# Optimization experiments

Measured on AMD Instinct MI355X. Metric: run time of the kernel, lower is better.

The kernel has to match this reference:

```python
import jax, jax.numpy as jnp
import numpy as np

N = 20000
E = 320000
D = 256
OUT = 256
NEG_SLOPE = 0.2


def setup_inputs() -> dict:
    key = jax.random.key(0)
    ks = jax.random.split(key, 16)
    s = 1.0 / np.sqrt(D)
    x = jax.random.normal(ks[0], (N, D), dtype=jnp.float32)
    edge_index = jax.random.randint(ks[1], (2, E), 0, N, dtype=jnp.int64)
    W1 = jax.random.uniform(ks[2], (D, D), jnp.float32, -s, s)
    W2 = jax.random.uniform(ks[3], (D, D), jnp.float32, -s, s)
    Ws = jax.random.uniform(ks[4], (6, D, D), jnp.float32, -s, s)      # per-layer GATConv lin weight
    a_src = jax.random.uniform(ks[5], (6, D), jnp.float32, -s, s)      # per-layer att_src
    a_dst = jax.random.uniform(ks[6], (6, D), jnp.float32, -s, s)      # per-layer att_dst
    bias = jnp.zeros((6, D), dtype=jnp.float32)                        # per-layer GATConv bias
    W3 = jax.random.uniform(ks[7], (2 * D, OUT), jnp.float32, -s, s)
    return {"x": x, "edge_index": edge_index, "W1": W1, "W2": W2,
            "Ws": Ws, "a_src": a_src, "a_dst": a_dst, "bias": bias, "W3": W3}


def _gat_layer(h, src, dst, W, asrc, adst, b):
    # h: [N, D] -> linear transform
    hw = h @ W                                         # [N, D]
    e_src = hw @ asrc                                  # [N]
    e_dst = hw @ adst                                  # [N]
    e = jax.nn.leaky_relu(e_src[src] + e_dst[dst], NEG_SLOPE)  # [E]
    # softmax over incoming edges per destination node
    m = jax.ops.segment_max(e, dst, num_segments=N)    # [N], -inf for empty segs (unused)
    ee = jnp.exp(e - m[dst])                           # [E]
    denom = jax.ops.segment_sum(ee, dst, num_segments=N)
    alpha = ee / denom[dst]                            # [E]
    msg = alpha[:, None] * hw[src]                     # [E, D]
    out = jax.ops.segment_sum(msg, dst, num_segments=N)  # [N, D]
    return out + b


def reference(x, edge_index, W1, W2, Ws, a_src, a_dst, bias, W3):
    src, dst = edge_index[0], edge_index[1]
    h = x @ W1
    h = h @ W2
    for i in range(6):
        h = _gat_layer(h, src, dst, Ws[i], a_src[i], a_dst[i], bias[i])
    h = jnp.concatenate((h, h), axis=1)   # [N, 2D]
    h = jax.nn.relu(h)
    return h @ W3                          # [N, OUT]
```

## Files before the change

kernel.cpp:

```cpp
#include <hip/hip_runtime.h>
#include <hip/hip_fp16.h>
#include <stdint.h>

#define NNODES 20000
#define EEDGES 320000
#define DD     256
#define NEG_SLOPE 0.2f
#define SCAN_BLOCKS ((NNODES + 255) / 256)
#define ESTR   20480

typedef _Float16 half8 __attribute__((ext_vector_type(8)));
typedef _Float16 half4 __attribute__((ext_vector_type(4)));
typedef float f32x4 __attribute__((ext_vector_type(4)));


__global__ void zero_ints_k(int* __restrict__ p, int n) {
    int i = blockIdx.x * 256 + threadIdx.x;
    if (i < n) p[i] = 0;
}

__global__ void hist_k(const int* __restrict__ dst, int* __restrict__ rowptr) {
    int i = blockIdx.x * 256 + threadIdx.x;
    if (i < EEDGES) atomicAdd(&rowptr[dst[i] + 1], 1);
}

__global__ __launch_bounds__(256) void scan1_k(int* __restrict__ rowptr, int* __restrict__ bsums) {
    __shared__ int buf[256];
    int idx = blockIdx.x * 256 + threadIdx.x;
    int v = (idx < NNODES) ? rowptr[idx + 1] : 0;
    buf[threadIdx.x] = v;
    __syncthreads();
#pragma unroll
    for (int off = 1; off < 256; off <<= 1) {
        int t = (threadIdx.x >= (unsigned)off) ? buf[threadIdx.x - off] : 0;
        __syncthreads();
        buf[threadIdx.x] += t;
        __syncthreads();
    }
    if (idx < NNODES) rowptr[idx + 1] = buf[threadIdx.x];
    if (threadIdx.x == 255) bsums[blockIdx.x] = buf[255];
}

__global__ __launch_bounds__(128) void scan2_k(int* __restrict__ bsums) {
    __shared__ int buf[128];
    int v = (threadIdx.x < SCAN_BLOCKS) ? bsums[threadIdx.x] : 0;
    buf[threadIdx.x] = v;
    __syncthreads();
#pragma unroll
    for (int off = 1; off < 128; off <<= 1) {
        int t = (threadIdx.x >= (unsigned)off) ? buf[threadIdx.x - off] : 0;
        __syncthreads();
        buf[threadIdx.x] += t;
        __syncthreads();
    }
    if (threadIdx.x < SCAN_BLOCKS) bsums[threadIdx.x] = buf[threadIdx.x];
}

__global__ void scan3_k(int* __restrict__ rowptr, const int* __restrict__ bsums,
                        int* __restrict__ cursor) {
    int idx = blockIdx.x * 256 + threadIdx.x;
    if (idx < NNODES) {
        int v = rowptr[idx + 1];
        if (blockIdx.x > 0) { v += bsums[blockIdx.x - 1]; rowptr[idx + 1] = v; }
        if (idx + 1 < NNODES) cursor[idx + 1] = v;
        if (idx == 0) cursor[0] = 0;
    }
}

__global__ void scatter_k(const int* __restrict__ src, const int* __restrict__ dst,
                          int* __restrict__ cursor, int* __restrict__ colsrc) {
    int i = blockIdx.x * 256 + threadIdx.x;
    if (i < EEDGES) {
        int d = dst[i];
        int pos = atomicAdd(&cursor[d], 1);
        colsrc[pos] = src[i];
    }
}


__global__ void cvt_split_k(const float* __restrict__ X, _Float16* __restrict__ Xh,
                            _Float16* __restrict__ Xl, int n) {
    int i = blockIdx.x * 256 + threadIdx.x;
    if (i < n) {
        float v = X[i];
        _Float16 hi = (_Float16)v;
        Xh[i] = hi;
        Xl[i] = (_Float16)(v - (float)hi);
    }
}


template<bool SUM>
__global__ void cvt_w_k(const float* __restrict__ W, _Float16* __restrict__ Wh,
                        _Float16* __restrict__ Wl) {
    int i = blockIdx.x * 256 + threadIdx.x;
    if (i < DD * DD) {
        int k = i >> 8, n = i & 255;
        float v = W[i];
        if (SUM) v += W[i + DD * DD];
        _Float16 hi = (_Float16)v;
        Wh[n * DD + k] = hi;
        Wl[n * DD + k] = (_Float16)(v - (float)hi);
    }
}


template<bool OUT_SPLIT, bool DOTS>
__global__ __launch_bounds__(512, 4) void gemm_k(
    const _Float16* __restrict__ Ah, const _Float16* __restrict__ Al,
    const _Float16* __restrict__ Bh, const _Float16* __restrict__ Bl,
    float* __restrict__ C, _Float16* __restrict__ Ch, _Float16* __restrict__ Cl,
    const float* __restrict__ asrc, const float* __restrict__ adst,
    float* __restrict__ esp, float* __restrict__ edp, int M)
{
    __shared__ _Float16 smem[24576];
    _Float16* sAh = smem;
    _Float16* sAl = smem + 4096;
    _Float16* sBh = smem + 8192;
    _Float16* sBl = smem + 16384;

    const int t = threadIdx.x;
    const int lane = t & 63;
    const int w = t >> 6;
    const int rowBase = blockIdx.y * 64;
    const int colBase = blockIdx.x * 128;
    const int mo = (w & 1) * 32;
    const int no = (w >> 1) * 32;

    const int arow = t >> 3;
    const int slot = t & 7;
    const int swz = (slot ^ (arow & 7)) << 3;

    f32x4 acc[2][2];
#pragma unroll
    for (int m = 0; m < 2; ++m)
#pragma unroll
        for (int n = 0; n < 2; ++n) acc[m][n] = (f32x4){0.f, 0.f, 0.f, 0.f};

    int4 pa_h, pa_l, pb_h0, pb_h1, pb_l0, pb_l1;

#define LOADSTAGE(S) { \
        size_t aoff  = (size_t)(rowBase + arow) * DD + (S) * 64 + slot * 8; \
        size_t boff0 = (size_t)(colBase + arow) * DD + (S) * 64 + slot * 8; \
        size_t boff1 = boff0 + (size_t)64 * DD; \
        pa_h  = *(const int4*)(Ah + aoff); \
        pa_l  = *(const int4*)(Al + aoff); \
        pb_h0 = *(const int4*)(Bh + boff0); \
        pb_h1 = *(const int4*)(Bh + boff1); \
        pb_l0 = *(const int4*)(Bl + boff0); \
        pb_l1 = *(const int4*)(Bl + boff1); \
    }

#define WRITESTAGE() { \
        int da  = arow * 64 + swz; \
        *(int4*)(sAh + da) = pa_h; \
        *(int4*)(sAl + da) = pa_l; \
        *(int4*)(sBh + da) = pb_h0; \
        *(int4*)(sBh + da + 4096) = pb_h1; \
        *(int4*)(sBl + da) = pb_l0; \
        *(int4*)(sBl + da + 4096) = pb_l1; \
    }

    LOADSTAGE(0);
    const int fr = lane & 15;
    const int fq = lane >> 4;

    for (int s = 0; s < 4; ++s) {
        __syncthreads();
        WRITESTAGE();
        __syncthreads();
        if (s < 3) { LOADSTAGE(s + 1); }

#pragma unroll
        for (int kk = 0; kk < 2; ++kk) {
            const int c = kk * 4 + fq;
            half8 ah[2], al[2], bh[2], bl[2];
#pragma unroll
            for (int m = 0; m < 2; ++m) {
                int ra = mo + m * 16 + fr;
                int oa = ra * 64 + ((c ^ (ra & 7)) << 3);
                ah[m] = *(const half8*)(sAh + oa);
                al[m] = *(const half8*)(sAl + oa);
            }
#pragma unroll
            for (int n = 0; n < 2; ++n) {
                int rb = no + n * 16 + fr;
                int ob = rb * 64 + ((c ^ (rb & 7)) << 3);
                bh[n] = *(const half8*)(sBh + ob);
                bl[n] = *(const half8*)(sBl + ob);
            }
#pragma unroll
            for (int m = 0; m < 2; ++m)
#pragma unroll
                for (int n = 0; n < 2; ++n) {
                    acc[m][n] = __builtin_amdgcn_mfma_f32_16x16x32_f16(ah[m], bh[n], acc[m][n], 0, 0, 0);
                    acc[m][n] = __builtin_amdgcn_mfma_f32_16x16x32_f16(ah[m], bl[n], acc[m][n], 0, 0, 0);
                    acc[m][n] = __builtin_amdgcn_mfma_f32_16x16x32_f16(al[m], bh[n], acc[m][n], 0, 0, 0);
                    acc[m][n] = __builtin_amdgcn_mfma_f32_16x16x32_f16(al[m], bl[n], acc[m][n], 0, 0, 0);
                }
        }
    }
#undef LOADSTAGE
#undef WRITESTAGE

    const int ccol = lane & 15;
    const int crq = (lane >> 4) * 4;

    if constexpr (OUT_SPLIT) {
        __syncthreads();
#pragma unroll
        for (int m = 0; m < 2; ++m)
#pragma unroll
            for (int n = 0; n < 2; ++n)
#pragma unroll
                for (int r = 0; r < 4; ++r) {
                    int row = mo + m * 16 + crq + r;
                    int col = no + n * 16 + ccol;
                    float v = acc[m][n][r];
                    _Float16 hi = (_Float16)v;
                    smem[row * 136 + col] = hi;
                    smem[8704 + row * 136 + col] = (_Float16)(v - (float)hi);
                }
        __syncthreads();
#pragma unroll
        for (int i = 0; i < 2; ++i) {
            int slotId = i * 512 + t;
            int srow = slotId >> 4;
            int sc = slotId & 15;
            int grow = rowBase + srow;
            if (grow < M) {
                half8 hv = *(const half8*)(smem + srow * 136 + sc * 8);
                half8 lv = *(const half8*)(smem + 8704 + srow * 136 + sc * 8);
                *(half8*)(Ch + (size_t)grow * DD + colBase + sc * 8) = hv;
                *(half8*)(Cl + (size_t)grow * DD + colBase + sc * 8) = lv;
            }
        }
    } else {
#pragma unroll
        for (int m = 0; m < 2; ++m) {
            int growb = rowBase + mo + m * 16 + crq;
#pragma unroll
            for (int n = 0; n < 2; ++n) {
                int gcol = colBase + no + n * 16 + ccol;
#pragma unroll
                for (int r = 0; r < 4; ++r) {
                    int grow = growb + r;
                    if (grow < M) C[(size_t)grow * DD + gcol] = acc[m][n][r];
                }
            }
        }
    }

    if constexpr (DOTS) {
        float as0 = asrc[colBase + no + ccol];
        float as1 = asrc[colBase + no + 16 + ccol];
        float ad0 = adst[colBase + no + ccol];
        float ad1 = adst[colBase + no + 16 + ccol];
        __syncthreads();
        float* sred = (float*)smem;
        const int cw = w >> 1;
#pragma unroll
        for (int m = 0; m < 2; ++m)
#pragma unroll
            for (int r = 0; r < 4; ++r) {
                float ps = acc[m][0][r] * as0 + acc[m][1][r] * as1;
                float pd = acc[m][0][r] * ad0 + acc[m][1][r] * ad1;
#pragma unroll
                for (int off = 1; off < 16; off <<= 1) {
                    ps += __shfl_xor(ps, off);
                    pd += __shfl_xor(pd, off);
                }
                if (ccol == 0) {
                    int row = mo + m * 16 + crq + r;
                    sred[row * 8 + cw] = ps;
                    sred[512 + row * 8 + cw] = pd;
                }
            }
        __syncthreads();
        if (t < 64) {
            float esb = sred[t * 8 + 0] + sred[t * 8 + 1] + sred[t * 8 + 2] + sred[t * 8 + 3];
            float edb = sred[512 + t * 8 + 0] + sred[512 + t * 8 + 1]
                      + sred[512 + t * 8 + 2] + sred[512 + t * 8 + 3];
            int grow = rowBase + t;
            if (grow < M) {
                esp[(size_t)blockIdx.x * ESTR + grow] = esb;
                edp[(size_t)blockIdx.x * ESTR + grow] = edb;
            }
        }
    }
}


template<bool RELU>
__global__ __launch_bounds__(256) void gat_agg_k(const float* __restrict__ hw,
                                                 const float* __restrict__ es0,
                                                 const float* __restrict__ es1,
                                                 const float* __restrict__ ed0,
                                                 const float* __restrict__ ed1,
                                                 const int* __restrict__ rowptr,
                                                 const int* __restrict__ colsrc,
                                                 float* __restrict__ ealpha,
                                                 const float* __restrict__ bias,
                                                 _Float16* __restrict__ hh,
                                                 _Float16* __restrict__ hl) {
    int wave = threadIdx.x >> 6;
    int lane = threadIdx.x & 63;
    int node = blockIdx.x * 4 + wave;
    if (node >= NNODES) return;
    int start = rowptr[node], end = rowptr[node + 1];
    int deg = end - start;
    float edd = ed0[node] + ed1[node];

    float4 acc0 = make_float4(0.f, 0.f, 0.f, 0.f);
    float4 acc1 = acc0, acc2 = acc0, acc3 = acc0;
    float4 acc4 = acc0, acc5 = acc0, acc6 = acc0, acc7 = acc0;

#define FMA4(ACC, W_, V) \
    ACC.x = fmaf(W_, V.x, ACC.x); ACC.y = fmaf(W_, V.y, ACC.y); \
    ACC.z = fmaf(W_, V.z, ACC.z); ACC.w = fmaf(W_, V.w, ACC.w);

    if (deg <= 64) {
        if (deg > 0) {
            int j = start + lane;
            bool valid = j < end;
            int msrc = valid ? colsrc[j] : 0;
            float e = valid ? es0[msrc] + es1[msrc] + edd : -INFINITY;
            e = fmaxf(e, NEG_SLOPE * e);
            float mx = e;
#pragma unroll
            for (int off = 32; off; off >>= 1) mx = fmaxf(mx, __shfl_xor(mx, off));
            float ee = valid ? expf(e - mx) : 0.f;
            float sum = ee;
#pragma unroll
            for (int off = 32; off; off >>= 1) sum += __shfl_xor(sum, off);
            float w = ee / sum;

            int j2 = 0;
            for (; j2 + 8 <= deg; j2 += 8) {
                int s0 = __shfl(msrc, j2 + 0), s1 = __shfl(msrc, j2 + 1);
                int s2 = __shfl(msrc, j2 + 2), s3 = __shfl(msrc, j2 + 3);
                int s4 = __shfl(msrc, j2 + 4), s5 = __shfl(msrc, j2 + 5);
                int s6 = __shfl(msrc, j2 + 6), s7 = __shfl(msrc, j2 + 7);
                float w0 = __shfl(w, j2 + 0), w1 = __shfl(w, j2 + 1);
                float w2 = __shfl(w, j2 + 2), w3 = __shfl(w, j2 + 3);
                float w4 = __shfl(w, j2 + 4), w5 = __shfl(w, j2 + 5);
                float w6 = __shfl(w, j2 + 6), w7 = __shfl(w, j2 + 7);
                float4 v0 = *(const float4*)(hw + (size_t)s0 * DD + lane * 4);
                float4 v1 = *(const float4*)(hw + (size_t)s1 * DD + lane * 4);
                float4 v2 = *(const float4*)(hw + (size_t)s2 * DD + lane * 4);
                float4 v3 = *(const float4*)(hw + (size_t)s3 * DD + lane * 4);
                float4 v4 = *(const float4*)(hw + (size_t)s4 * DD + lane * 4);
                float4 v5 = *(const float4*)(hw + (size_t)s5 * DD + lane * 4);
                float4 v6 = *(const float4*)(hw + (size_t)s6 * DD + lane * 4);
                float4 v7 = *(const float4*)(hw + (size_t)s7 * DD + lane * 4);
                FMA4(acc0, w0, v0); FMA4(acc1, w1, v1);
                FMA4(acc2, w2, v2); FMA4(acc3, w3, v3);
                FMA4(acc4, w4, v4); FMA4(acc5, w5, v5);
                FMA4(acc6, w6, v6); FMA4(acc7, w7, v7);
            }
            if (j2 + 4 <= deg) {
                int s0 = __shfl(msrc, j2 + 0), s1 = __shfl(msrc, j2 + 1);
                int s2 = __shfl(msrc, j2 + 2), s3 = __shfl(msrc, j2 + 3);
                float w0 = __shfl(w, j2 + 0), w1 = __shfl(w, j2 + 1);
                float w2 = __shfl(w, j2 + 2), w3 = __shfl(w, j2 + 3);
                float4 v0 = *(const float4*)(hw + (size_t)s0 * DD + lane * 4);
                float4 v1 = *(const float4*)(hw + (size_t)s1 * DD + lane * 4);
                float4 v2 = *(const float4*)(hw + (size_t)s2 * DD + lane * 4);
                float4 v3 = *(const float4*)(hw + (size_t)s3 * DD + lane * 4);
                FMA4(acc0, w0, v0); FMA4(acc1, w1, v1);
                FMA4(acc2, w2, v2); FMA4(acc3, w3, v3);
                j2 += 4;
            }
            for (; j2 < deg; ++j2) {
                int   s0 = __shfl(msrc, j2);
                float w0 = __shfl(w, j2);
                float4 v0 = *(const float4*)(hw + (size_t)s0 * DD + lane * 4);
                FMA4(acc0, w0, v0);
            }
        }
    } else {
        float mx = -INFINITY;
        for (int j = start + lane; j < end; j += 64) {
            int s = colsrc[j];
            float e = es0[s] + es1[s] + edd;
            e = fmaxf(e, NEG_SLOPE * e);
            mx = fmaxf(mx, e);
        }
#pragma unroll
        for (int off = 32; off; off >>= 1) mx = fmaxf(mx, __shfl_xor(mx, off));
        float sum = 0.f;
        for (int j = start + lane; j < end; j += 64) {
            int s = colsrc[j];
            float e = es0[s] + es1[s] + edd;
            e = fmaxf(e, NEG_SLOPE * e);
            float ee = expf(e - mx);
            ealpha[j] = ee;
            sum += ee;
        }
#pragma unroll
        for (int off = 32; off; off >>= 1) sum += __shfl_xor(sum, off);
        float inv = 1.f / sum;
        int j = start;
        for (; j + 4 <= end; j += 4) {
            int s0 = colsrc[j], s1 = colsrc[j + 1], s2 = colsrc[j + 2], s3 = colsrc[j + 3];
            float w0 = ealpha[j] * inv, w1 = ealpha[j + 1] * inv;
            float w2 = ealpha[j + 2] * inv, w3 = ealpha[j + 3] * inv;
            float4 v0 = *(const float4*)(hw + (size_t)s0 * DD + lane * 4);
            float4 v1 = *(const float4*)(hw + (size_t)s1 * DD + lane * 4);
            float4 v2 = *(const float4*)(hw + (size_t)s2 * DD + lane * 4);
            float4 v3 = *(const float4*)(hw + (size_t)s3 * DD + lane * 4);
            FMA4(acc0, w0, v0); FMA4(acc1, w1, v1);
            FMA4(acc2, w2, v2); FMA4(acc3, w3, v3);
        }
        for (; j < end; ++j) {
            int s0 = colsrc[j];
            float w0 = ealpha[j] * inv;
            float4 v0 = *(const float4*)(hw + (size_t)s0 * DD + lane * 4);
            FMA4(acc0, w0, v0);
        }
    }
#undef FMA4

    acc0.x += acc4.x; acc0.y += acc4.y; acc0.z += acc4.z; acc0.w += acc4.w;
    acc1.x += acc5.x; acc1.y += acc5.y; acc1.z += acc5.z; acc1.w += acc5.w;
    acc2.x += acc6.x; acc2.y += acc6.y; acc2.z += acc6.z; acc2.w += acc6.w;
    acc3.x += acc7.x; acc3.y += acc7.y; acc3.z += acc7.z; acc3.w += acc7.w;
    acc0.x += acc1.x; acc0.y += acc1.y; acc0.z += acc1.z; acc0.w += acc1.w;
    acc2.x += acc3.x; acc2.y += acc3.y; acc2.z += acc3.z; acc2.w += acc3.w;
    acc0.x += acc2.x; acc0.y += acc2.y; acc0.z += acc2.z; acc0.w += acc2.w;
    float4 b4 = *(const float4*)(bias + lane * 4);
    acc0.x += b4.x; acc0.y += b4.y; acc0.z += b4.z; acc0.w += b4.w;
    if (RELU) {
        acc0.x = fmaxf(acc0.x, 0.f); acc0.y = fmaxf(acc0.y, 0.f);
        acc0.z = fmaxf(acc0.z, 0.f); acc0.w = fmaxf(acc0.w, 0.f);
    }
    size_t base = (size_t)node * DD + lane * 4;
    _Float16 h0 = (_Float16)acc0.x, h1 = (_Float16)acc0.y;
    _Float16 h2 = (_Float16)acc0.z, h3 = (_Float16)acc0.w;
    half4 hv; hv[0] = h0; hv[1] = h1; hv[2] = h2; hv[3] = h3;
    half4 lv;
    lv[0] = (_Float16)(acc0.x - (float)h0); lv[1] = (_Float16)(acc0.y - (float)h1);
    lv[2] = (_Float16)(acc0.z - (float)h2); lv[3] = (_Float16)(acc0.w - (float)h3);
    *(half4*)(hh + base) = hv;
    *(half4*)(hl + base) = lv;
}


extern "C" void kernel_launch(void* const* d_in, const int* in_sizes, int n_in,
                              void* d_out, int out_size, void* d_ws, size_t ws_size,
                              hipStream_t stream) {
    const float* x     = (const float*)d_in[0];
    const int*   ei    = (const int*)d_in[1];
    const float* W1    = (const float*)d_in[2];
    const float* W2    = (const float*)d_in[3];
    const float* Ws    = (const float*)d_in[4];
    const float* a_src = (const float*)d_in[5];
    const float* a_dst = (const float*)d_in[6];
    const float* bias  = (const float*)d_in[7];
    const float* W3    = (const float*)d_in[8];
    float* out = (float*)d_out;

    const int* src = ei;
    const int* dst = ei + EEDGES;

    const size_t ND = (size_t)NNODES * DD;

    float* bufA   = (float*)d_ws;
    float* es01   = bufA + ND;
    float* ed01   = es01 + 2 * ESTR;
    float* ealpha = ed01 + 2 * ESTR;
    int*   rowptr = (int*)(ealpha + EEDGES);
    int*   cursor = rowptr + (NNODES + 1);
    int*   colsrc = cursor + NNODES;
    int*   bsums  = colsrc + EEDGES;
    _Float16* P0h = (_Float16*)(((uintptr_t)(bsums + SCAN_BLOCKS) + 15) & ~(uintptr_t)15);
    _Float16* P0l = P0h + ND;
    _Float16* P1h = P0l + ND;
    _Float16* P1l = P1h + ND;
    _Float16* WT  = P1l + ND;
    const size_t WSZ = (size_t)DD * DD;

#define WTH(i) (WT + (i) * 2 * WSZ)
#define WTL(i) (WT + (i) * 2 * WSZ + WSZ)

    zero_ints_k<<<(NNODES + 1 + 255) / 256, 256, 0, stream>>>(rowptr, NNODES + 1);
    hist_k<<<(EEDGES + 255) / 256, 256, 0, stream>>>(dst, rowptr);
    scan1_k<<<SCAN_BLOCKS, 256, 0, stream>>>(rowptr, bsums);
    scan2_k<<<1, 128, 0, stream>>>(bsums);
    scan3_k<<<SCAN_BLOCKS, 256, 0, stream>>>(rowptr, bsums, cursor);
    scatter_k<<<(EEDGES + 255) / 256, 256, 0, stream>>>(src, dst, cursor, colsrc);

    const int WBLK = (DD * DD + 255) / 256;
    cvt_split_k<<<WBLK, 256, 0, stream>>>(W1, WTH(0), WTL(0), DD * DD);
    cvt_w_k<false><<<WBLK, 256, 0, stream>>>(W2, WTH(1), WTL(1));
    for (int l = 0; l < 6; ++l)
        cvt_w_k<false><<<WBLK, 256, 0, stream>>>(Ws + (size_t)l * WSZ, WTH(2 + l), WTL(2 + l));
    cvt_w_k<true><<<WBLK, 256, 0, stream>>>(W3, WTH(8), WTL(8));

    dim3 gw(DD / 128, (DD + 63) / 64);
    gemm_k<true, false><<<gw, 512, 0, stream>>>(WTH(1), WTL(1), WTH(0), WTL(0),
                                                nullptr, WTH(9), WTL(9),
                                                nullptr, nullptr, nullptr, nullptr, DD);

    cvt_split_k<<<(int)((ND + 255) / 256), 256, 0, stream>>>(x, P0h, P0l, (int)ND);

    dim3 gg(DD / 128, (NNODES + 63) / 64);
    const int nodeBlocks = (NNODES + 3) / 4;

    gemm_k<true, false><<<gg, 512, 0, stream>>>(P0h, P0l, WTH(9), WTL(9), nullptr, P1h, P1l,
                                                nullptr, nullptr, nullptr, nullptr, NNODES);

    for (int l = 0; l < 6; ++l) {
        gemm_k<false, true><<<gg, 512, 0, stream>>>(P1h, P1l, WTH(2 + l), WTL(2 + l),
                                                    bufA, nullptr, nullptr,
                                                    a_src + (size_t)l * DD, a_dst + (size_t)l * DD,
                                                    es01, ed01, NNODES);
        if (l < 5)
            gat_agg_k<false><<<nodeBlocks, 256, 0, stream>>>(bufA, es01, es01 + ESTR,
                                                             ed01, ed01 + ESTR,
                                                             rowptr, colsrc, ealpha,
                                                             bias + (size_t)l * DD, P1h, P1l);
        else
            gat_agg_k<true><<<nodeBlocks, 256, 0, stream>>>(bufA, es01, es01 + ESTR,
                                                            ed01, ed01 + ESTR,
                                                            rowptr, colsrc, ealpha,
                                                            bias + (size_t)l * DD, P1h, P1l);
    }

    gemm_k<false, false><<<gg, 512, 0, stream>>>(P1h, P1l, WTH(8), WTL(8), out,
                                                 nullptr, nullptr,
                                                 nullptr, nullptr, nullptr, nullptr, NNODES);
#undef WTH
#undef WTL
}
```

Baseline: 596.3 us.

## Split GAT aggregation across two waves per node, remap GEMM blocks per XCD, fuse weight conversion

The aggregation kernel now uses two waves per destination node. Each wave handles alternating 8-edge chunks, and the two partial sums are combined through shared memory, which doubles the parallelism available to hide gather latency. The GEMM grid is flattened to 1D and block ids are remapped so that consecutive row tiles land on the same XCD, aiming for better L2 reuse of A tiles. The separate weight conversion launches are merged into one launch with a 2D grid. The trade-off is an added __syncthreads, and high-degree nodes are still processed by a single wave, which may leave its partner wave idle.

```diff
diff --git a/kernel.cpp b/kernel.cpp
--- a/kernel.cpp
+++ b/kernel.cpp
@@ -90,14 +90,25 @@
 }
 
 
-template<bool SUM>
-__global__ void cvt_w_k(const float* __restrict__ W, _Float16* __restrict__ Wh,
-                        _Float16* __restrict__ Wl) {
+__global__ void cvt_weights_k(const float* __restrict__ W1, const float* __restrict__ W2,
+                              const float* __restrict__ Ws, const float* __restrict__ W3,
+                              _Float16* __restrict__ WT) {
     int i = blockIdx.x * 256 + threadIdx.x;
-    if (i < DD * DD) {
+    if (i >= DD * DD) return;
+    const size_t WSZ = (size_t)DD * DD;
+    int y = blockIdx.y;
+    _Float16* Wh = WT + (size_t)y * 2 * WSZ;
+    _Float16* Wl = Wh + WSZ;
+    if (y == 0) {
+        float v = W1[i];
+        _Float16 hi = (_Float16)v;
+        Wh[i] = hi;
+        Wl[i] = (_Float16)(v - (float)hi);
+    } else {
+        const float* W = (y == 1) ? W2 : (y == 8) ? W3 : (Ws + (size_t)(y - 2) * WSZ);
         int k = i >> 8, n = i & 255;
         float v = W[i];
-        if (SUM) v += W[i + DD * DD];
+        if (y == 8) v += W3[i + WSZ];
         _Float16 hi = (_Float16)v;
         Wh[n * DD + k] = hi;
         Wl[n * DD + k] = (_Float16)(v - (float)hi);
@@ -113,6 +124,14 @@
     const float* __restrict__ asrc, const float* __restrict__ adst,
     float* __restrict__ esp, float* __restrict__ edp, int M)
 {
+    const int nwg = gridDim.x;
+    const int orig = blockIdx.x;
+    const int q = nwg >> 3, r = nwg & 7;
+    const int xcd = orig & 7, idx = orig >> 3;
+    const int sw = (xcd < r ? xcd * (q + 1) : r * (q + 1) + (xcd - r) * q) + idx;
+    const int by = sw >> 1;
+    const int bx = sw & 1;
+
     __shared__ _Float16 smem[24576];
     _Float16* sAh = smem;
     _Float16* sAl = smem + 4096;
@@ -122,8 +141,8 @@
     const int t = threadIdx.x;
     const int lane = t & 63;
     const int w = t >> 6;
-    const int rowBase = blockIdx.y * 64;
-    const int colBase = blockIdx.x * 128;
+    const int rowBase = by * 64;
+    const int colBase = bx * 128;
     const int mo = (w & 1) * 32;
     const int no = (w >> 1) * 32;
 
@@ -283,8 +302,8 @@
                       + sred[512 + t * 8 + 2] + sred[512 + t * 8 + 3];
             int grow = rowBase + t;
             if (grow < M) {
-                esp[(size_t)blockIdx.x * ESTR + grow] = esb;
-                edp[(size_t)blockIdx.x * ESTR + grow] = edb;
+                esp[(size_t)bx * ESTR + grow] = esb;
+                edp[(size_t)bx * ESTR + grow] = edb;
             }
         }
     }
@@ -292,7 +311,7 @@
 
 
 template<bool RELU>
-__global__ __launch_bounds__(256) void gat_agg_k(const float* __restrict__ hw,
+__global__ __launch_bounds__(512) void gat_agg_k(const float* __restrict__ hw,
                                                  const float* __restrict__ es0,
                                                  const float* __restrict__ es1,
                                                  const float* __restrict__ ed0,
@@ -303,10 +322,14 @@
                                                  const float* __restrict__ bias,
                                                  _Float16* __restrict__ hh,
                                                  _Float16* __restrict__ hl) {
-    int wave = threadIdx.x >> 6;
-    int lane = threadIdx.x & 63;
-    int node = blockIdx.x * 4 + wave;
-    if (node >= NNODES) return;
+    __shared__ float sacc[4][DD];
+    const int t = threadIdx.x;
+    const int lane = t & 63;
+    const int wv = t >> 6;
+    const int ni = wv >> 1;
+    const int h  = wv & 1;
+    const int node = blockIdx.x * 4 + ni;
+
     int start = rowptr[node], end = rowptr[node + 1];
     int deg = end - start;
     float edd = ed0[node] + ed1[node];
@@ -319,32 +342,31 @@
     ACC.x = fmaf(W_, V.x, ACC.x); ACC.y = fmaf(W_, V.y, ACC.y); \
     ACC.z = fmaf(W_, V.z, ACC.z); ACC.w = fmaf(W_, V.w, ACC.w);
 
-    if (deg <= 64) {
-        if (deg > 0) {
-            int j = start + lane;
-            bool valid = j < end;
-            int msrc = valid ? colsrc[j] : 0;
-            float e = valid ? es0[msrc] + es1[msrc] + edd : -INFINITY;
-            e = fmaxf(e, NEG_SLOPE * e);
-            float mx = e;
-#pragma unroll
-            for (int off = 32; off; off >>= 1) mx = fmaxf(mx, __shfl_xor(mx, off));
-            float ee = valid ? expf(e - mx) : 0.f;
-            float sum = ee;
-#pragma unroll
-            for (int off = 32; off; off >>= 1) sum += __shfl_xor(sum, off);
-            float w = ee / sum;
-
-            int j2 = 0;
-            for (; j2 + 8 <= deg; j2 += 8) {
-                int s0 = __shfl(msrc, j2 + 0), s1 = __shfl(msrc, j2 + 1);
-                int s2 = __shfl(msrc, j2 + 2), s3 = __shfl(msrc, j2 + 3);
-                int s4 = __shfl(msrc, j2 + 4), s5 = __shfl(msrc, j2 + 5);
-                int s6 = __shfl(msrc, j2 + 6), s7 = __shfl(msrc, j2 + 7);
-                float w0 = __shfl(w, j2 + 0), w1 = __shfl(w, j2 + 1);
-                float w2 = __shfl(w, j2 + 2), w3 = __shfl(w, j2 + 3);
-                float w4 = __shfl(w, j2 + 4), w5 = __shfl(w, j2 + 5);
-                float w6 = __shfl(w, j2 + 6), w7 = __shfl(w, j2 + 7);
+    if (deg > 0 && deg <= 64) {
+        int j = start + lane;
+        bool valid = j < end;
+        int msrc = valid ? colsrc[j] : 0;
+        float e = valid ? es0[msrc] + es1[msrc] + edd : -INFINITY;
+        e = fmaxf(e, NEG_SLOPE * e);
+        float mx = e;
+#pragma unroll
+        for (int off = 32; off; off >>= 1) mx = fmaxf(mx, __shfl_xor(mx, off));
+        float ee = valid ? expf(e - mx) : 0.f;
+        float sum = ee;
+#pragma unroll
+        for (int off = 32; off; off >>= 1) sum += __shfl_xor(sum, off);
+        float w = ee / sum;
+
+        for (int b = h * 8; b < deg; b += 16) {
+            if (deg - b >= 8) {
+                int s0 = __shfl(msrc, b + 0), s1 = __shfl(msrc, b + 1);
+                int s2 = __shfl(msrc, b + 2), s3 = __shfl(msrc, b + 3);
+                int s4 = __shfl(msrc, b + 4), s5 = __shfl(msrc, b + 5);
+                int s6 = __shfl(msrc, b + 6), s7 = __shfl(msrc, b + 7);
+                float w0 = __shfl(w, b + 0), w1 = __shfl(w, b + 1);
+                float w2 = __shfl(w, b + 2), w3 = __shfl(w, b + 3);
+                float w4 = __shfl(w, b + 4), w5 = __shfl(w, b + 5);
+                float w6 = __shfl(w, b + 6), w7 = __shfl(w, b + 7);
                 float4 v0 = *(const float4*)(hw + (size_t)s0 * DD + lane * 4);
                 float4 v1 = *(const float4*)(hw + (size_t)s1 * DD + lane * 4);
                 float4 v2 = *(const float4*)(hw + (size_t)s2 * DD + lane * 4);
@@ -357,28 +379,30 @@
                 FMA4(acc2, w2, v2); FMA4(acc3, w3, v3);
                 FMA4(acc4, w4, v4); FMA4(acc5, w5, v5);
                 FMA4(acc6, w6, v6); FMA4(acc7, w7, v7);
-            }
-            if (j2 + 4 <= deg) {
-                int s0 = __shfl(msrc, j2 + 0), s1 = __shfl(msrc, j2 + 1);
-                int s2 = __shfl(msrc, j2 + 2), s3 = __shfl(msrc, j2 + 3);
-                float w0 = __shfl(w, j2 + 0), w1 = __shfl(w, j2 + 1);
-                float w2 = __shfl(w, j2 + 2), w3 = __shfl(w, j2 + 3);
-                float4 v0 = *(const float4*)(hw + (size_t)s0 * DD + lane * 4);
-                float4 v1 = *(const float4*)(hw + (size_t)s1 * DD + lane * 4);
-                float4 v2 = *(const float4*)(hw + (size_t)s2 * DD + lane * 4);
-                float4 v3 = *(const float4*)(hw + (size_t)s3 * DD + lane * 4);
-                FMA4(acc0, w0, v0); FMA4(acc1, w1, v1);
-                FMA4(acc2, w2, v2); FMA4(acc3, w3, v3);
-                j2 += 4;
-            }
-            for (; j2 < deg; ++j2) {
-                int   s0 = __shfl(msrc, j2);
-                float w0 = __shfl(w, j2);
-                float4 v0 = *(const float4*)(hw + (size_t)s0 * DD + lane * 4);
-                FMA4(acc0, w0, v0);
-            }
-        }
-    } else {
+            } else {
+                int j2 = b;
+                if (j2 + 4 <= deg) {
+                    int s0 = __shfl(msrc, j2 + 0), s1 = __shfl(msrc, j2 + 1);
+                    int s2 = __shfl(msrc, j2 + 2), s3 = __shfl(msrc, j2 + 3);
+                    float w0 = __shfl(w, j2 + 0), w1 = __shfl(w, j2 + 1);
+                    float w2 = __shfl(w, j2 + 2), w3 = __shfl(w, j2 + 3);
+                    float4 v0 = *(const float4*)(hw + (size_t)s0 * DD + lane * 4);
+                    float4 v1 = *(const float4*)(hw + (size_t)s1 * DD + lane * 4);
+                    float4 v2 = *(const float4*)(hw + (size_t)s2 * DD + lane * 4);
+                    float4 v3 = *(const float4*)(hw + (size_t)s3 * DD + lane * 4);
+                    FMA4(acc0, w0, v0); FMA4(acc1, w1, v1);
+                    FMA4(acc2, w2, v2); FMA4(acc3, w3, v3);
+                    j2 += 4;
+                }
+                for (; j2 < deg; ++j2) {
+                    int   s0 = __shfl(msrc, j2);
+                    float w0 = __shfl(w, j2);
+                    float4 v0 = *(const float4*)(hw + (size_t)s0 * DD + lane * 4);
+                    FMA4(acc0, w0, v0);
+                }
+            }
+        }
+    } else if (deg > 64 && h == 0) {
         float mx = -INFINITY;
         for (int j = start + lane; j < end; j += 64) {
             int s = colsrc[j];
@@ -428,21 +452,28 @@
     acc0.x += acc1.x; acc0.y += acc1.y; acc0.z += acc1.z; acc0.w += acc1.w;
     acc2.x += acc3.x; acc2.y += acc3.y; acc2.z += acc3.z; acc2.w += acc3.w;
     acc0.x += acc2.x; acc0.y += acc2.y; acc0.z += acc2.z; acc0.w += acc2.w;
-    float4 b4 = *(const float4*)(bias + lane * 4);
-    acc0.x += b4.x; acc0.y += b4.y; acc0.z += b4.z; acc0.w += b4.w;
-    if (RELU) {
-        acc0.x = fmaxf(acc0.x, 0.f); acc0.y = fmaxf(acc0.y, 0.f);
-        acc0.z = fmaxf(acc0.z, 0.f); acc0.w = fmaxf(acc0.w, 0.f);
-    }
-    size_t base = (size_t)node * DD + lane * 4;
-    _Float16 h0 = (_Float16)acc0.x, h1 = (_Float16)acc0.y;
-    _Float16 h2 = (_Float16)acc0.z, h3 = (_Float16)acc0.w;
-    half4 hv; hv[0] = h0; hv[1] = h1; hv[2] = h2; hv[3] = h3;
-    half4 lv;
-    lv[0] = (_Float16)(acc0.x - (float)h0); lv[1] = (_Float16)(acc0.y - (float)h1);
-    lv[2] = (_Float16)(acc0.z - (float)h2); lv[3] = (_Float16)(acc0.w - (float)h3);
-    *(half4*)(hh + base) = hv;
-    *(half4*)(hl + base) = lv;
+
+    if (h == 1) *(float4*)&sacc[ni][lane * 4] = acc0;
+    __syncthreads();
+    if (h == 0) {
+        float4 o = *(const float4*)&sacc[ni][lane * 4];
+        acc0.x += o.x; acc0.y += o.y; acc0.z += o.z; acc0.w += o.w;
+        float4 b4 = *(const float4*)(bias + lane * 4);
+        acc0.x += b4.x; acc0.y += b4.y; acc0.z += b4.z; acc0.w += b4.w;
+        if (RELU) {
+            acc0.x = fmaxf(acc0.x, 0.f); acc0.y = fmaxf(acc0.y, 0.f);
+            acc0.z = fmaxf(acc0.z, 0.f); acc0.w = fmaxf(acc0.w, 0.f);
+        }
+        size_t base = (size_t)node * DD + lane * 4;
+        _Float16 h0 = (_Float16)acc0.x, h1 = (_Float16)acc0.y;
+        _Float16 h2 = (_Float16)acc0.z, h3 = (_Float16)acc0.w;
+        half4 hv; hv[0] = h0; hv[1] = h1; hv[2] = h2; hv[3] = h3;
+        half4 lv;
+        lv[0] = (_Float16)(acc0.x - (float)h0); lv[1] = (_Float16)(acc0.y - (float)h1);
+        lv[2] = (_Float16)(acc0.z - (float)h2); lv[3] = (_Float16)(acc0.w - (float)h3);
+        *(half4*)(hh + base) = hv;
+        *(half4*)(hl + base) = lv;
+    }
 }
 
 
@@ -491,43 +522,38 @@
     scatter_k<<<(EEDGES + 255) / 256, 256, 0, stream>>>(src, dst, cursor, colsrc);
 
     const int WBLK = (DD * DD + 255) / 256;
-    cvt_split_k<<<WBLK, 256, 0, stream>>>(W1, WTH(0), WTL(0), DD * DD);
-    cvt_w_k<false><<<WBLK, 256, 0, stream>>>(W2, WTH(1), WTL(1));
-    for (int l = 0; l < 6; ++l)
-        cvt_w_k<false><<<WBLK, 256, 0, stream>>>(Ws + (size_t)l * WSZ, WTH(2 + l), WTL(2 + l));
-    cvt_w_k<true><<<WBLK, 256, 0, stream>>>(W3, WTH(8), WTL(8));
-
-    dim3 gw(DD / 128, (DD + 63) / 64);
-    gemm_k<true, false><<<gw, 512, 0, stream>>>(WTH(1), WTL(1), WTH(0), WTL(0),
-                                                nullptr, WTH(9), WTL(9),
-                                                nullptr, nullptr, nullptr, nullptr, DD);
+    cvt_weights_k<<<dim3(WBLK, 9), 256, 0, stream>>>(W1, W2, Ws, W3, WT);
+
+    gemm_k<true, false><<<8, 512, 0, stream>>>(WTH(1), WTL(1), WTH(0), WTL(0),
+                                               nullptr, WTH(9), WTL(9),
+                                               nullptr, nullptr, nullptr, nullptr, DD);
 
     cvt_split_k<<<(int)((ND + 255) / 256), 256, 0, stream>>>(x, P0h, P0l, (int)ND);
 
-    dim3 gg(DD / 128, (NNODES + 63) / 64);
+    const int GG = 2 * ((NNODES + 63) / 64);
     const int nodeBlocks = (NNODES + 3) / 4;
 
-    gemm_k<true, false><<<gg, 512, 0, stream>>>(P0h, P0l, WTH(9), WTL(9), nullptr, P1h, P1l,
+    gemm_k<true, false><<<GG, 512, 0, stream>>>(P0h, P0l, WTH(9), WTL(9), nullptr, P1h, P1l,
                                                 nullptr, nullptr, nullptr, nullptr, NNODES);
 
     for (int l = 0; l < 6; ++l) {
-        gemm_k<false, true><<<gg, 512, 0, stream>>>(P1h, P1l, WTH(2 + l), WTL(2 + l),
+        gemm_k<false, true><<<GG, 512, 0, stream>>>(P1h, P1l, WTH(2 + l), WTL(2 + l),
                                                     bufA, nullptr, nullptr,
                                                     a_src + (size_t)l * DD, a_dst + (size_t)l * DD,
                                                     es01, ed01, NNODES);
         if (l < 5)
-            gat_agg_k<false><<<nodeBlocks, 256, 0, stream>>>(bufA, es01, es01 + ESTR,
+            gat_agg_k<false><<<nodeBlocks, 512, 0, stream>>>(bufA, es01, es01 + ESTR,
                                                              ed01, ed01 + ESTR,
                                                              rowptr, colsrc, ealpha,
                                                              bias + (size_t)l * DD, P1h, P1l);
         else
-            gat_agg_k<true><<<nodeBlocks, 256, 0, stream>>>(bufA, es01, es01 + ESTR,
+            gat_agg_k<true><<<nodeBlocks, 512, 0, stream>>>(bufA, es01, es01 + ESTR,
                                                             ed01, ed01 + ESTR,
                                                             rowptr, colsrc, ealpha,
                                                             bias + (size_t)l * DD, P1h, P1l);
     }
 
-    gemm_k<false, false><<<gg, 512, 0, stream>>>(P1h, P1l, WTH(8), WTL(8), out,
+    gemm_k<false, false><<<GG, 512, 0, stream>>>(P1h, P1l, WTH(8), WTL(8), out,
                                                  nullptr, nullptr,
                                                  nullptr, nullptr, nullptr, nullptr, NNODES);
 #undef WTH
```

Measured after the change: 596.9 us. About the same (+0.1%).
